# Kernel tuning notes

Measured on AMD Instinct MI355X. Metric: run time of the kernel, lower is better.

Reference implementation:

```python
import jax, jax.numpy as jnp
import numpy as np

# ST-GCN spatial graph convolution:
#   f = Conv2d_1x1(x)                       -> [N, K*C_out, T, V]
#   f = reshape to [N, K, C_out, T, V]
#   out[n,c,t,w] = sum_{k,v} f[n,k,c,t,v] * A[k,v,w]

N, C_IN, T, V = 32, 64, 300, 25
K, C_OUT = 3, 64


def setup_inputs() -> dict:
    key = jax.random.key(0)
    k1, k2, k3, k4 = jax.random.split(key, 4)
    x = jax.random.normal(k1, (N, C_IN, T, V), dtype=jnp.float32)
    W = jax.random.normal(k2, (K * C_OUT, C_IN), dtype=jnp.float32) * 0.05  # 1x1 conv weight
    b = jax.random.normal(k3, (K * C_OUT,), dtype=jnp.float32) * 0.05
    # Normalized adjacency stack [K, V, V] (row-normalized random graph, stands in
    # for adj.normalize(create_adjacency_matrices(strat)))
    A = jax.random.uniform(k4, (K, V, V), dtype=jnp.float32)
    A = A / jnp.sum(A, axis=-1, keepdims=True)
    return {"x": x, "W": W, "b": b, "A": A}


def reference(x, W, b, A):
    # 1x1 conv == per-(t,v) channel projection
    f = jnp.einsum("nctv,oc->notv", x, W) + b[None, :, None, None]  # [N, K*C_out, T, V]
    f = f.reshape(N, K, C_OUT, T, V)
    # adjacency-weighted neighbor aggregation
    out = jnp.einsum("nkctv,kvw->nctw", f, A)  # [N, C_out, T, V]
    return out
```

## Files before the change

kernel.cpp:

```cpp
#include <hip/hip_runtime.h>
#include <hip/hip_bf16.h>


#define CIN   64
#define T_    300
#define V_    25
#define COUT  64

#define WS_W2 0
#define WS_AH 24576
#define WS_BO 49152
#define WS_BYTES 57344

#define LDS_W2 0
#define LDS_AH 24576
#define LDS_BO 49152
#define SMEM_BYTES 57344

typedef short  bf16x8 __attribute__((ext_vector_type(8)));
typedef float  f32x4  __attribute__((ext_vector_type(4)));

__device__ __forceinline__ unsigned short cvt_bf16(float f) {
    union { __hip_bfloat16 h; unsigned short u; } cv;
    cv.h = __float2bfloat16(f);
    return cv.u;
}
__device__ __forceinline__ unsigned pk2(float a, float b) {
    return (unsigned)cvt_bf16(a) | ((unsigned)cvt_bf16(b) << 16);
}
union fragu { bf16x8 v; unsigned u[4]; };

#define GLL16(g, s) __builtin_amdgcn_global_load_lds( \
    (const __attribute__((address_space(1))) void*)(g), \
    (__attribute__((address_space(3))) void*)(s), 16, 0, 0)

__global__ void gcn_prep(const float* __restrict__ W, const float* __restrict__ bias,
                         const float* __restrict__ A, unsigned char* __restrict__ ws)
{
    const int tid = blockIdx.x * 256 + threadIdx.x;
    for (int i = tid; i < 4 * 6 * 64 * 8; i += 4096) {
        const int e = i & 7, lane = (i >> 3) & 63, ck = i >> 9;
        const int kap = ck % 6, ct = ck / 6;
        const int lr = lane & 15, lq = lane >> 4;
        const int row = (kap >> 1) * COUT + ct * 16 + lr;
        const int col = 32 * (kap & 1) + 16 * (e >> 2) + 4 * lq + (e & 3);
        reinterpret_cast<unsigned short*>(ws + WS_W2)[i] = cvt_bf16(W[row * CIN + col]);
    }
    for (int i = tid; i < 4 * 96 * 32; i += 4096) {
        const int vp = i & 31, kw = (i >> 5) % 96, dd = (i >> 5) / 96;
        const int k = kw >> 5, w = kw & 31, v = vp - dd;
        const float val = (v >= 0 && v < V_ && w < V_) ? A[(k * V_ + v) * V_ + w] : 0.f;
        reinterpret_cast<unsigned short*>(ws + WS_AH)[i] = cvt_bf16(val);
    }
    for (int i = tid; i < 32 * 64; i += 4096) {
        const int w = i >> 6, c = i & 63;
        float s = 0.f;
        if (w < V_) {
            for (int k = 0; k < 3; ++k) {
                float sa = 0.f;
                for (int v = 0; v < V_; ++v) sa += A[(k * V_ + v) * V_ + w];
                s += bias[k * COUT + c] * sa;
            }
        }
        reinterpret_cast<float*>(ws + WS_BO)[i] = s;
    }
}

__global__ __launch_bounds__(1024, 4) void gcn_main(
    const float* __restrict__ x, const unsigned char* __restrict__ ws,
    float* __restrict__ out)
{
    __shared__ __align__(16) unsigned char smem[SMEM_BYTES];

    const int tid = threadIdx.x;
    const int wv = tid >> 6, l = tid & 63, lr = l & 15, lq = l >> 4;
    const int gid = blockIdx.x * 16 + wv;
    const int n = gid / T_, t = gid % T_;
    const int d = t & 3;
    const int qoff = t * V_ - d;

    const float* xrow = x + (size_t)(n * CIN + lr) * (T_ * V_) + qoff + 8 * lq;
    f32x4 xa[4], xg[4];
    #pragma unroll
    for (int mi = 0; mi < 4; ++mi) {
        const float* p = xrow + (size_t)mi * 16 * (T_ * V_);
        xa[mi] = *reinterpret_cast<const f32x4*>(p);
        xg[mi] = *reinterpret_cast<const f32x4*>(p + (lq < 3 ? 4 : 0));
    }

    for (int s = wv; s < 56; s += 16) {
        const unsigned char* src;
        if (s < 24) {
            src = ws + WS_W2 + s * 1024 + l * 16;
        } else if (s < 48) {
            src = ws + WS_AH + (s - 24) * 1024 + 64 * lr + 16 * lq;
        } else {
            const int i2 = s - 48, nt = i2 & 1, ct = i2 >> 1;
            src = ws + WS_BO + (16 * nt + lr) * 256 + 64 * ct + 16 * lq;
        }
        GLL16(src, smem + s * 1024);
    }
    __builtin_amdgcn_sched_barrier(0);

    bf16x8 xf[4];
    #pragma unroll
    for (int mi = 0; mi < 4; ++mi) {
        fragu f;
        f.u[0] = pk2(xa[mi][0], xa[mi][1]);
        f.u[1] = pk2(xa[mi][2], xa[mi][3]);
        f.u[2] = pk2(xg[mi][0], xg[mi][1]);
        f.u[3] = pk2(xg[mi][2], xg[mi][3]);
        xf[mi] = f.v;
    }

    __syncthreads();

    f32x4 oacc[4][2];
    #pragma unroll
    for (int ct = 0; ct < 4; ++ct)
        #pragma unroll
        for (int nt = 0; nt < 2; ++nt)
            oacc[ct][nt] = *reinterpret_cast<const f32x4*>(
                smem + LDS_BO + ((ct * 2 + nt) << 10) + l * 16);

    #pragma unroll
    for (int k = 0; k < 3; ++k) {
        bf16x8 ahf[2];
        #pragma unroll
        for (int j = 0; j < 2; ++j)
            ahf[j] = *reinterpret_cast<const bf16x8*>(
                smem + LDS_AH + ((d * 6 + 2 * k + j) << 10) + l * 16);

        f32x4 y[4][2];
        #pragma unroll
        for (int mi = 0; mi < 4; ++mi)
            #pragma unroll
            for (int j = 0; j < 2; ++j)
                y[mi][j] = (f32x4){0.f, 0.f, 0.f, 0.f};
        #pragma unroll
        for (int j = 0; j < 2; ++j)
            #pragma unroll
            for (int mi = 0; mi < 4; ++mi)
                y[mi][j] = __builtin_amdgcn_mfma_f32_16x16x32_bf16(
                    xf[mi], ahf[j], y[mi][j], 0, 0, 0);

        #pragma unroll
        for (int kl = 0; kl < 2; ++kl) {
            bf16x8 w2f[4];
            #pragma unroll
            for (int ct = 0; ct < 4; ++ct)
                w2f[ct] = *reinterpret_cast<const bf16x8*>(
                    smem + LDS_W2 + ((ct * 6 + 2 * k + kl) << 10) + l * 16);
            #pragma unroll
            for (int nt = 0; nt < 2; ++nt) {
                fragu bb;
                bb.u[0] = pk2(y[2 * kl][nt][0],     y[2 * kl][nt][1]);
                bb.u[1] = pk2(y[2 * kl][nt][2],     y[2 * kl][nt][3]);
                bb.u[2] = pk2(y[2 * kl + 1][nt][0], y[2 * kl + 1][nt][1]);
                bb.u[3] = pk2(y[2 * kl + 1][nt][2], y[2 * kl + 1][nt][3]);
                #pragma unroll
                for (int ct = 0; ct < 4; ++ct)
                    oacc[ct][nt] = __builtin_amdgcn_mfma_f32_16x16x32_bf16(
                        w2f[ct], bb.v, oacc[ct][nt], 0, 0, 0);
            }
        }
    }

    float* ob = out + ((size_t)(n * COUT) * T_ + t) * V_;
    #pragma unroll
    for (int ct = 0; ct < 4; ++ct) {
        #pragma unroll
        for (int r = 0; r < 4; ++r) {
            const int c = 16 * ct + 4 * lq + r;
            float* op = ob + (size_t)c * (T_ * V_);
            op[lr] = oacc[ct][0][r];
            if (lr < 9) op[16 + lr] = oacc[ct][1][r];
        }
    }
}

extern "C" void kernel_launch(void* const* d_in, const int* in_sizes, int n_in,
                              void* d_out, int out_size, void* d_ws, size_t ws_size,
                              hipStream_t stream) {
    const float* x    = (const float*)d_in[0];
    const float* W    = (const float*)d_in[1];
    const float* bias = (const float*)d_in[2];
    const float* A    = (const float*)d_in[3];
    float* out = (float*)d_out;
    unsigned char* ws = (unsigned char*)d_ws;

    hipLaunchKernelGGL(gcn_prep, dim3(16), dim3(256), 0, stream, W, bias, A, ws);
    hipLaunchKernelGGL(gcn_main, dim3(600), dim3(1024), 0, stream, x, ws, out);
}
```

Baseline: 42.96 us.

## Make main kernel persistent with software-pipelined x loads across items

Replaces one-item-per-wave with a grid of 512 blocks of 8 waves (4096 waves), each processing two or three (n,t) items. The x loads for the next items are issued before the current item's MFMA work, so global latency overlaps compute. The shared W/A/bias staging into LDS is now paid once per block for more items. The cost is extra registers for double-buffered x fragments and uneven work, since some waves handle three items and others two.

```diff
diff --git a/kernel.cpp b/kernel.cpp
--- a/kernel.cpp
+++ b/kernel.cpp
@@ -6,6 +6,8 @@
 #define T_    300
 #define V_    25
 #define COUT  64
+#define NITEM 9600
+#define NWAVE 4096
 
 #define WS_W2 0
 #define WS_AH 24576
@@ -66,7 +68,7 @@
     }
 }
 
-__global__ __launch_bounds__(1024, 4) void gcn_main(
+__global__ __launch_bounds__(512, 4) void gcn_main(
     const float* __restrict__ x, const unsigned char* __restrict__ ws,
     float* __restrict__ out)
 {
@@ -74,21 +76,95 @@
 
     const int tid = threadIdx.x;
     const int wv = tid >> 6, l = tid & 63, lr = l & 15, lq = l >> 4;
-    const int gid = blockIdx.x * 16 + wv;
-    const int n = gid / T_, t = gid % T_;
-    const int d = t & 3;
-    const int qoff = t * V_ - d;
-
-    const float* xrow = x + (size_t)(n * CIN + lr) * (T_ * V_) + qoff + 8 * lq;
-    f32x4 xa[4], xg[4];
-    #pragma unroll
-    for (int mi = 0; mi < 4; ++mi) {
-        const float* p = xrow + (size_t)mi * 16 * (T_ * V_);
-        xa[mi] = *reinterpret_cast<const f32x4*>(p);
-        xg[mi] = *reinterpret_cast<const f32x4*>(p + (lq < 3 ? 4 : 0));
-    }
-
-    for (int s = wv; s < 56; s += 16) {
+    const int wid = blockIdx.x * 8 + wv;
+
+    auto loadx = [&](int it, f32x4 (&xa)[4], f32x4 (&xg)[4]) {
+        const int n = it / T_, t = it % T_, d = t & 3;
+        const float* xrow = x + (size_t)(n * CIN + lr) * (T_ * V_) + (t * V_ - d) + 8 * lq;
+        #pragma unroll
+        for (int mi = 0; mi < 4; ++mi) {
+            const float* p = xrow + (size_t)mi * 16 * (T_ * V_);
+            xa[mi] = *reinterpret_cast<const f32x4*>(p);
+            xg[mi] = *reinterpret_cast<const f32x4*>(p + (lq < 3 ? 4 : 0));
+        }
+    };
+    auto cvtx = [&](f32x4 (&xa)[4], f32x4 (&xg)[4], bf16x8 (&xf)[4]) {
+        #pragma unroll
+        for (int mi = 0; mi < 4; ++mi) {
+            fragu f;
+            f.u[0] = pk2(xa[mi][0], xa[mi][1]);
+            f.u[1] = pk2(xa[mi][2], xa[mi][3]);
+            f.u[2] = pk2(xg[mi][0], xg[mi][1]);
+            f.u[3] = pk2(xg[mi][2], xg[mi][3]);
+            xf[mi] = f.v;
+        }
+    };
+    auto process = [&](int it, bf16x8 (&xf)[4]) {
+        const int n = it / T_, t = it % T_, d = t & 3;
+        f32x4 oacc[4][2];
+        #pragma unroll
+        for (int ct = 0; ct < 4; ++ct)
+            #pragma unroll
+            for (int nt = 0; nt < 2; ++nt)
+                oacc[ct][nt] = *reinterpret_cast<const f32x4*>(
+                    smem + LDS_BO + ((ct * 2 + nt) << 10) + l * 16);
+        #pragma unroll
+        for (int k = 0; k < 3; ++k) {
+            bf16x8 ahf[2];
+            #pragma unroll
+            for (int j = 0; j < 2; ++j)
+                ahf[j] = *reinterpret_cast<const bf16x8*>(
+                    smem + LDS_AH + ((d * 6 + 2 * k + j) << 10) + l * 16);
+            f32x4 y[4][2];
+            #pragma unroll
+            for (int mi = 0; mi < 4; ++mi)
+                #pragma unroll
+                for (int j = 0; j < 2; ++j)
+                    y[mi][j] = (f32x4){0.f, 0.f, 0.f, 0.f};
+            #pragma unroll
+            for (int j = 0; j < 2; ++j)
+                #pragma unroll
+                for (int mi = 0; mi < 4; ++mi)
+                    y[mi][j] = __builtin_amdgcn_mfma_f32_16x16x32_bf16(
+                        xf[mi], ahf[j], y[mi][j], 0, 0, 0);
+            #pragma unroll
+            for (int kl = 0; kl < 2; ++kl) {
+                bf16x8 w2f[4];
+                #pragma unroll
+                for (int ct = 0; ct < 4; ++ct)
+                    w2f[ct] = *reinterpret_cast<const bf16x8*>(
+                        smem + LDS_W2 + ((ct * 6 + 2 * k + kl) << 10) + l * 16);
+                #pragma unroll
+                for (int nt = 0; nt < 2; ++nt) {
+                    fragu bb;
+                    bb.u[0] = pk2(y[2 * kl][nt][0],     y[2 * kl][nt][1]);
+                    bb.u[1] = pk2(y[2 * kl][nt][2],     y[2 * kl][nt][3]);
+                    bb.u[2] = pk2(y[2 * kl + 1][nt][0], y[2 * kl + 1][nt][1]);
+                    bb.u[3] = pk2(y[2 * kl + 1][nt][2], y[2 * kl + 1][nt][3]);
+                    #pragma unroll
+                    for (int ct = 0; ct < 4; ++ct)
+                        oacc[ct][nt] = __builtin_amdgcn_mfma_f32_16x16x32_bf16(
+                            w2f[ct], bb.v, oacc[ct][nt], 0, 0, 0);
+                }
+            }
+        }
+        float* ob = out + ((size_t)(n * COUT) * T_ + t) * V_;
+        #pragma unroll
+        for (int ct = 0; ct < 4; ++ct) {
+            #pragma unroll
+            for (int r = 0; r < 4; ++r) {
+                const int c = 16 * ct + 4 * lq + r;
+                float* op = ob + (size_t)c * (T_ * V_);
+                op[lr] = oacc[ct][0][r];
+                if (lr < 9) op[16 + lr] = oacc[ct][1][r];
+            }
+        }
+    };
+
+    f32x4 xa0[4], xg0[4], xa1[4], xg1[4];
+    loadx(wid, xa0, xg0);
+
+    for (int s = wv; s < 56; s += 8) {
         const unsigned char* src;
         if (s < 24) {
             src = ws + WS_W2 + s * 1024 + l * 16;
@@ -101,81 +177,24 @@
         GLL16(src, smem + s * 1024);
     }
     __builtin_amdgcn_sched_barrier(0);
+    __syncthreads();
+
+    loadx(wid + NWAVE, xa1, xg1);
+    __builtin_amdgcn_sched_barrier(0);
 
     bf16x8 xf[4];
-    #pragma unroll
-    for (int mi = 0; mi < 4; ++mi) {
-        fragu f;
-        f.u[0] = pk2(xa[mi][0], xa[mi][1]);
-        f.u[1] = pk2(xa[mi][2], xa[mi][3]);
-        f.u[2] = pk2(xg[mi][0], xg[mi][1]);
-        f.u[3] = pk2(xg[mi][2], xg[mi][3]);
-        xf[mi] = f.v;
-    }
-
-    __syncthreads();
-
-    f32x4 oacc[4][2];
-    #pragma unroll
-    for (int ct = 0; ct < 4; ++ct)
-        #pragma unroll
-        for (int nt = 0; nt < 2; ++nt)
-            oacc[ct][nt] = *reinterpret_cast<const f32x4*>(
-                smem + LDS_BO + ((ct * 2 + nt) << 10) + l * 16);
-
-    #pragma unroll
-    for (int k = 0; k < 3; ++k) {
-        bf16x8 ahf[2];
-        #pragma unroll
-        for (int j = 0; j < 2; ++j)
-            ahf[j] = *reinterpret_cast<const bf16x8*>(
-                smem + LDS_AH + ((d * 6 + 2 * k + j) << 10) + l * 16);
-
-        f32x4 y[4][2];
-        #pragma unroll
-        for (int mi = 0; mi < 4; ++mi)
-            #pragma unroll
-            for (int j = 0; j < 2; ++j)
-                y[mi][j] = (f32x4){0.f, 0.f, 0.f, 0.f};
-        #pragma unroll
-        for (int j = 0; j < 2; ++j)
-            #pragma unroll
-            for (int mi = 0; mi < 4; ++mi)
-                y[mi][j] = __builtin_amdgcn_mfma_f32_16x16x32_bf16(
-                    xf[mi], ahf[j], y[mi][j], 0, 0, 0);
-
-        #pragma unroll
-        for (int kl = 0; kl < 2; ++kl) {
-            bf16x8 w2f[4];
-            #pragma unroll
-            for (int ct = 0; ct < 4; ++ct)
-                w2f[ct] = *reinterpret_cast<const bf16x8*>(
-                    smem + LDS_W2 + ((ct * 6 + 2 * k + kl) << 10) + l * 16);
-            #pragma unroll
-            for (int nt = 0; nt < 2; ++nt) {
-                fragu bb;
-                bb.u[0] = pk2(y[2 * kl][nt][0],     y[2 * kl][nt][1]);
-                bb.u[1] = pk2(y[2 * kl][nt][2],     y[2 * kl][nt][3]);
-                bb.u[2] = pk2(y[2 * kl + 1][nt][0], y[2 * kl + 1][nt][1]);
-                bb.u[3] = pk2(y[2 * kl + 1][nt][2], y[2 * kl + 1][nt][3]);
-                #pragma unroll
-                for (int ct = 0; ct < 4; ++ct)
-                    oacc[ct][nt] = __builtin_amdgcn_mfma_f32_16x16x32_bf16(
-                        w2f[ct], bb.v, oacc[ct][nt], 0, 0, 0);
-            }
-        }
-    }
-
-    float* ob = out + ((size_t)(n * COUT) * T_ + t) * V_;
-    #pragma unroll
-    for (int ct = 0; ct < 4; ++ct) {
-        #pragma unroll
-        for (int r = 0; r < 4; ++r) {
-            const int c = 16 * ct + 4 * lq + r;
-            float* op = ob + (size_t)c * (T_ * V_);
-            op[lr] = oacc[ct][0][r];
-            if (lr < 9) op[16 + lr] = oacc[ct][1][r];
-        }
+    cvtx(xa0, xg0, xf);
+    const bool has2 = wid + 2 * NWAVE < NITEM;
+    if (has2) loadx(wid + 2 * NWAVE, xa0, xg0);
+    __builtin_amdgcn_sched_barrier(0);
+    process(wid, xf);
+
+    cvtx(xa1, xg1, xf);
+    process(wid + NWAVE, xf);
+
+    if (has2) {
+        cvtx(xa0, xg0, xf);
+        process(wid + 2 * NWAVE, xf);
     }
 }
 
@@ -190,5 +209,5 @@
     unsigned char* ws = (unsigned char*)d_ws;
 
     hipLaunchKernelGGL(gcn_prep, dim3(16), dim3(256), 0, stream, W, bias, A, ws);
-    hipLaunchKernelGGL(gcn_main, dim3(600), dim3(1024), 0, stream, x, ws, out);
-}
+    hipLaunchKernelGGL(gcn_main, dim3(512), dim3(512), 0, stream, x, ws, out);
+}
```

Result: slower. 45.83 us (+6.7%).
